# Kernel tuning notes

Measured on AMD Instinct MI355X. Metric: run time of the kernel, lower is better.

The kernel has to match this reference:

```python
import jax, jax.numpy as jnp
import numpy as np

B, LV, HW, LT, D, H = 4, 16, 196, 32, 768, 12
DH = D // H
SCALE = 1.0 / np.sqrt(DH).astype(np.float32)


def _lin(x, W, b):
    # torch nn.Linear convention: W is [out, in]
    return x @ W.T + b


def _split_heads(x):
    # (..., D) -> (..., H, DH)
    return x.reshape(*x.shape[:-1], H, DH)


def _attn_logits(feat_q, feat_k, mask_q, mask_k, Wq, bq, Wk, bk):
    # feat_q: (B, LV, Lq, D), feat_k: (B, LV, Lk, D)
    q = _split_heads(_lin(feat_q, Wq, bq))  # b v q h d
    k = _split_heads(_lin(feat_k, Wk, bk))  # b v k h d
    logits = jnp.einsum('bvqhd,bvkhd->bvhqk', q, k)
    m = (mask_q[:, :, None] & mask_k[:, None, :])[:, None, None]  # b 1 1 q k
    return jnp.where(m, logits, -10000.0)


def setup_inputs() -> dict:
    key = jax.random.key(0)
    ks = jax.random.split(key, 12)
    inp = {
        'vid_feat': jax.random.normal(ks[0], (B, LV, HW, D), jnp.float32),
        'txt_feat': jax.random.normal(ks[1], (B, LV, LT, D), jnp.float32),
        'vid_mask': jnp.ones((B, LV), dtype=bool),
        'txt_mask': jax.random.randint(ks[2], (B, LT), 0, 2) > 0,
    }
    for i, name in enumerate(['v2v', 't2v', 't2t', 'v2t']):
        inp[name + '_W'] = jax.random.normal(ks[3 + 2 * i], (3, D, D), jnp.float32) * 0.02
        inp[name + '_b'] = jnp.zeros((3, D), jnp.float32)
    return inp


def reference(vid_feat, txt_feat, vid_mask, txt_mask,
              v2v_W, v2v_b, t2v_W, t2v_b, t2t_W, t2t_b, v2t_W, v2t_b):
    mask_hw = jnp.ones((vid_feat.shape[0], HW), dtype=bool)

    # values: concat video-keys then text-keys along the key axis
    v_value = jnp.concatenate([_lin(vid_feat, v2v_W[2], v2v_b[2]),
                               _lin(txt_feat, t2v_W[2], t2v_b[2])], axis=2)
    v_value = _split_heads(v_value)  # b v (HW+LT) h d
    t_value = jnp.concatenate([_lin(vid_feat, v2t_W[2], v2t_b[2]),
                               _lin(txt_feat, t2t_W[2], t2t_b[2])], axis=2)
    t_value = _split_heads(t_value)

    # logits (source call order: get_attn_logits(feat_k, mask_k, feat_q, mask_q, ...))
    v2v = _attn_logits(vid_feat, vid_feat, mask_hw, mask_hw, v2v_W[0], v2v_b[0], v2v_W[1], v2v_b[1])
    t2v = _attn_logits(vid_feat, txt_feat, mask_hw, txt_mask, t2v_W[0], t2v_b[0], t2v_W[1], t2v_b[1])
    v2t = _attn_logits(txt_feat, vid_feat, txt_mask, mask_hw, v2t_W[0], v2t_b[0], v2t_W[1], v2t_b[1])
    t2t = _attn_logits(txt_feat, txt_feat, txt_mask, txt_mask, t2t_W[0], t2t_b[0], t2t_W[1], t2t_b[1])

    v_logits = jnp.concatenate([v2v, t2v], axis=-1)  # b v h HW (HW+LT)
    t_logits = jnp.concatenate([v2t, t2t], axis=-1)  # b v h LT (HW+LT)

    # NOTE: source scales probabilities AFTER softmax by 1/sqrt(d_head)
    vid_out = jnp.einsum('bvhqk,bvkhd->bvqhd', jax.nn.softmax(v_logits, axis=-1) * SCALE, v_value)
    vid_out = vid_out.reshape(*vid_out.shape[:3], D)
    txt_out = jnp.einsum('bvhqk,bvkhd->bvqhd', jax.nn.softmax(t_logits, axis=-1) * SCALE, t_value)
    txt_out = txt_out.reshape(*txt_out.shape[:3], D)
    return (vid_out, txt_out)
```

## Files before the change

kernel.cpp:

```cpp
#include <hip/hip_runtime.h>

#define NBV 64
#define HWN 196
#define LTN 32
#define DIM 768
#define NH 12
#define DHD 64
#define ATT_SCALE 0.125f

typedef __attribute__((ext_vector_type(8))) __bf16 bf16x8;
typedef __attribute__((ext_vector_type(4))) float f32x4;

static __device__ __forceinline__ unsigned short f2bf(float f) {
    union { float f; unsigned u; } v; v.f = f;
    unsigned r = v.u + 0x7FFFu + ((v.u >> 16) & 1u);
    return (unsigned short)(r >> 16);
}

#define MFMA16(a, b, c) __builtin_amdgcn_mfma_f32_16x16x32_bf16((a), (b), (c), 0, 0, 0)
#define GLOAD_LDS16(g, l)                                                      \
    __builtin_amdgcn_global_load_lds(                                          \
        (const __attribute__((address_space(1))) void*)(g),                    \
        (__attribute__((address_space(3))) void*)(l), 16, 0, 0)

struct CvtCfg {
    const float* src[14];
    unsigned short* dst[14];
    int n4[14];
};

__global__ __launch_bounds__(256) void cvt_bf16(CvtCfg cfg) {
    const int e = blockIdx.y;
    const float4* s = (const float4*)cfg.src[e];
    unsigned short* d = cfg.dst[e];
    const int n4 = cfg.n4[e];
    for (int i = blockIdx.x * 256 + threadIdx.x; i < n4; i += gridDim.x * 256) {
        float4 v = s[i];
        ushort4 o;
        o.x = f2bf(v.x); o.y = f2bf(v.y); o.z = f2bf(v.z); o.w = f2bf(v.w);
        *(ushort4*)(d + (long)i * 4) = o;
    }
}

struct BiasCfg { const float* b[6]; };

__global__ __launch_bounds__(512, 2) void gemm_proj(
    const unsigned short* __restrict__ A, const unsigned short* __restrict__ W,
    unsigned short* __restrict__ out, BiasCfg bias, int M)
{
    __shared__ __align__(16) unsigned short lds[65536];
    const int tid = threadIdx.x;
    const int lane = tid & 63, wid = tid >> 6;
    const int wm = wid >> 2, wn = wid & 3;
    const int fr = lane & 15, fg = lane >> 4;

    const int nwg = gridDim.x;
    const int orig = blockIdx.x;
    const int q = nwg >> 3, r = nwg & 7;
    const int xcd = orig & 7, lid = orig >> 3;
    const int wg = (xcd < r ? xcd * (q + 1) : r * (q + 1) + (xcd - r) * q) + lid;
    const int mt = wg / 18, nt = wg - mt * 18;
    const int m0 = mt * 256, n0 = nt * 256;

    const int srow = tid >> 2;
    const int sxor = ((tid & 3) ^ ((tid >> 3) & 3)) * 8;
    const unsigned short* aSrc = A + (long)(m0 + srow) * DIM + sxor;
    const unsigned short* bSrc = W + (long)(n0 + srow) * DIM + sxor;
    unsigned short* ldst = lds + tid * 8;

    const int rxor = (fg ^ ((fr >> 1) & 3)) * 8;
    const int aoff = (wm * 128 + fr) * 32 + rxor;
    const int boff = 8192 + (wn * 64 + fr) * 32 + rxor;

    f32x4 acc[8][4] = {};

#define STAGE(t, s) do {                                                       \
    const unsigned short* _a = aSrc + (t) * 32;                                \
    const unsigned short* _b = bSrc + (t) * 32;                                \
    unsigned short* _d = ldst + (s) * 16384;                                   \
    GLOAD_LDS16(_a, _d);                                                       \
    GLOAD_LDS16(_a + 98304, _d + 4096);                                        \
    GLOAD_LDS16(_b, _d + 8192);                                                \
    GLOAD_LDS16(_b + 98304, _d + 12288);                                       \
} while (0)

#define COMPUTE(s) do {                                                        \
    const unsigned short* _sa = lds + (s) * 16384 + aoff;                      \
    const unsigned short* _sb = lds + (s) * 16384 + boff;                      \
    bf16x8 af[8], bg[4];                                                       \
    _Pragma("unroll") for (int m = 0; m < 8; ++m)                              \
        af[m] = *(const bf16x8*)(_sa + m * 512);                               \
    _Pragma("unroll") for (int n = 0; n < 4; ++n)                              \
        bg[n] = *(const bf16x8*)(_sb + n * 512);                               \
    __builtin_amdgcn_s_setprio(1);                                             \
    _Pragma("unroll") for (int m = 0; m < 8; ++m)                              \
    _Pragma("unroll") for (int n = 0; n < 4; ++n)                              \
        acc[m][n] = MFMA16(af[m], bg[n], acc[m][n]);                           \
    __builtin_amdgcn_s_setprio(0);                                             \
} while (0)

    STAGE(0, 0); STAGE(1, 1); STAGE(2, 2);
#pragma unroll 1
    for (int t = 0; t < 21; ++t) {
        STAGE(t + 3, (t + 3) & 3);
        asm volatile("s_waitcnt vmcnt(12)" ::: "memory");
        __builtin_amdgcn_s_barrier();
        COMPUTE(t & 3);
        __builtin_amdgcn_s_barrier();
    }
    asm volatile("s_waitcnt vmcnt(8)" ::: "memory");
    __builtin_amdgcn_s_barrier();
    COMPUTE(1);
    asm volatile("s_waitcnt vmcnt(4)" ::: "memory");
    __builtin_amdgcn_s_barrier();
    COMPUTE(2);
    asm volatile("s_waitcnt vmcnt(0)" ::: "memory");
    __builtin_amdgcn_s_barrier();
    COMPUTE(3);

#undef STAGE
#undef COMPUTE

    const int w = nt / 3;
    const int nlb = (nt - w * 3) * 256;
    const float* bp = bias.b[w];
    unsigned short* op = out + (long)w * M * DIM;
#pragma unroll
    for (int n = 0; n < 4; ++n) {
        int gn = nlb + wn * 64 + n * 16 + fr;
        float bvl = bp[gn];
#pragma unroll
        for (int m = 0; m < 8; ++m) {
            int gmb = m0 + wm * 128 + m * 16 + fg * 4;
#pragma unroll
            for (int j = 0; j < 4; ++j)
                op[(long)(gmb + j) * DIM + gn] = f2bf(acc[m][n][j] + bvl);
        }
    }
}

__global__ __launch_bounds__(256) void transpose_v(
    const unsigned short* __restrict__ src, unsigned short* __restrict__ dst,
    int nrows, int colbase)
{
    __shared__ unsigned short t[32][33];
    const int bv = blockIdx.z, rt = blockIdx.x, dt = blockIdx.y;
    const int tx = threadIdx.x & 31, ty = threadIdx.x >> 5;
#pragma unroll
    for (int i = 0; i < 4; ++i) {
        int r = rt * 32 + ty + i * 8;
        t[ty + i * 8][tx] = (r < nrows)
            ? src[(long)(bv * nrows + r) * DIM + dt * 32 + tx] : (unsigned short)0;
    }
    __syncthreads();
#pragma unroll
    for (int i = 0; i < 4; ++i) {
        int d = dt * 32 + ty + i * 8;
        int rr = rt * 32 + tx;
        if (rr < nrows)
            dst[(long)(bv * DIM + d) * 256 + colbase + rr] = t[tx][ty + i * 8];
    }
}

__global__ __launch_bounds__(256, 2) void attn_kernel(
    const unsigned short* __restrict__ QA, const unsigned short* __restrict__ QB,
    const unsigned short* __restrict__ KV, const unsigned short* __restrict__ KT,
    const unsigned short* __restrict__ Vt, const int* __restrict__ tmask,
    float* __restrict__ outp, int nq, int qmask)
{
    __shared__ __align__(16) unsigned short P[4][16][256];
    const int tid = threadIdx.x, lane = tid & 63, wid = tid >> 6;
    const int bv = blockIdx.x, h = blockIdx.y;
    const int b = bv >> 4;
    const int q0 = blockIdx.z * 64 + wid * 16;
    const int fr = lane & 15, fg = lane >> 4;

    int qr = q0 + fr; if (qr > nq - 1) qr = nq - 1;
    const unsigned short* qa_p = QA + (long)(bv * nq + qr) * DIM + h * DHD;
    const unsigned short* qb_p = QB + (long)(bv * nq + qr) * DIM + h * DHD;
    bf16x8 qa[2], qb[2];
#pragma unroll
    for (int kh = 0; kh < 2; ++kh) {
        qa[kh] = *(const bf16x8*)(qa_p + kh * 32 + fg * 8);
        qb[kh] = *(const bf16x8*)(qb_p + kh * 32 + fg * 8);
    }

    f32x4 acc[15];
#pragma unroll
    for (int kb = 0; kb < 13; ++kb) {
        int kr = kb * 16 + fr; if (kr > HWN - 1) kr = HWN - 1;
        const unsigned short* kp = KV + (long)(bv * HWN + kr) * DIM + h * DHD;
        f32x4 c = {0.f, 0.f, 0.f, 0.f};
        c = MFMA16(qa[0], *(const bf16x8*)(kp + fg * 8), c);
        c = MFMA16(qa[1], *(const bf16x8*)(kp + 32 + fg * 8), c);
        acc[kb] = c;
    }
#pragma unroll
    for (int kb = 13; kb < 15; ++kb) {
        int kr = (kb - 13) * 16 + fr;
        const unsigned short* kp = KT + (long)(bv * LTN + kr) * DIM + h * DHD;
        f32x4 c = {0.f, 0.f, 0.f, 0.f};
        c = MFMA16(qb[0], *(const bf16x8*)(kp + fg * 8), c);
        c = MFMA16(qb[1], *(const bf16x8*)(kp + 32 + fg * 8), c);
        acc[kb] = c;
    }

    bool vq[4];
#pragma unroll
    for (int j = 0; j < 4; ++j) {
        int q = q0 + fg * 4 + j;
        if (qmask) { int qc = q < LTN ? q : LTN - 1; vq[j] = tmask[b * LTN + qc] != 0; }
        else vq[j] = true;
    }
#pragma unroll
    for (int kb = 0; kb < 15; ++kb) {
        int c = kb * 16 + fr;
        bool kreal = (c < HWN) || (c >= 208);
        bool kvalid = true;
        if (c >= 208) kvalid = tmask[b * LTN + (c - 208)] != 0;
#pragma unroll
        for (int j = 0; j < 4; ++j) {
            float l = acc[kb][j];
            if (!kreal) l = -3.0e38f;
            else if (!(kvalid && vq[j])) l = -10000.0f;
            acc[kb][j] = l;
        }
    }

    float mx[4], sm[4];
#pragma unroll
    for (int j = 0; j < 4; ++j) {
        float m = acc[0][j];
#pragma unroll
        for (int kb = 1; kb < 15; ++kb) m = fmaxf(m, acc[kb][j]);
        for (int s = 1; s < 16; s <<= 1) m = fmaxf(m, __shfl_xor(m, s, 64));
        mx[j] = m;
    }
#pragma unroll
    for (int j = 0; j < 4; ++j) {
        float s = 0.f;
#pragma unroll
        for (int kb = 0; kb < 15; ++kb) {
            float p = __expf(acc[kb][j] - mx[j]);
            acc[kb][j] = p;
            s += p;
        }
        for (int st = 1; st < 16; st <<= 1) s += __shfl_xor(s, st, 64);
        sm[j] = s;
    }

#pragma unroll
    for (int kb = 0; kb < 15; ++kb)
#pragma unroll
        for (int j = 0; j < 4; ++j)
            P[wid][fg * 4 + j][kb * 16 + fr] = f2bf(acc[kb][j]);
#pragma unroll
    for (int j = 0; j < 4; ++j)
        P[wid][fg * 4 + j][240 + fr] = 0;
    __syncthreads();

    f32x4 oacc[4] = {};
    const unsigned short* vt_base = Vt + (long)(bv * DIM + h * DHD) * 256;
#pragma unroll
    for (int ks = 0; ks < 8; ++ks) {
        bf16x8 a = *(const bf16x8*)&P[wid][fr][ks * 32 + fg * 8];
#pragma unroll
        for (int n = 0; n < 4; ++n) {
            const unsigned short* vp = vt_base + (long)(n * 16 + fr) * 256 + ks * 32 + fg * 8;
            oacc[n] = MFMA16(a, *(const bf16x8*)vp, oacc[n]);
        }
    }

#pragma unroll
    for (int n = 0; n < 4; ++n)
#pragma unroll
        for (int j = 0; j < 4; ++j) {
            int q = q0 + fg * 4 + j;
            if (q < nq)
                outp[(long)(bv * nq + q) * DIM + h * DHD + n * 16 + fr] =
                    oacc[n][j] * (ATT_SCALE / sm[j]);
        }
}

extern "C" void kernel_launch(void* const* d_in, const int* in_sizes, int n_in,
                              void* d_out, int out_size, void* d_ws, size_t ws_size,
                              hipStream_t stream)
{
    const float* vid_feat = (const float*)d_in[0];
    const float* txt_feat = (const float*)d_in[1];
    const int*   txt_mask = (const int*)d_in[3];
    const float* v2v_W = (const float*)d_in[4];
    const float* v2v_b = (const float*)d_in[5];
    const float* t2v_W = (const float*)d_in[6];
    const float* t2v_b = (const float*)d_in[7];
    const float* t2t_W = (const float*)d_in[8];
    const float* t2t_b = (const float*)d_in[9];
    const float* v2t_W = (const float*)d_in[10];
    const float* v2t_b = (const float*)d_in[11];

    char* ws = (char*)d_ws;
    unsigned short* vid_bf   = (unsigned short*)(ws);
    unsigned short* txt_bf   = (unsigned short*)(ws + 19267584L);
    unsigned short* Wv_bf    = (unsigned short*)(ws + 22413312L);
    unsigned short* Wt_bf    = (unsigned short*)(ws + 29491200L);
    unsigned short* proj_vid = (unsigned short*)(ws + 36569088L);
    unsigned short* proj_txt = (unsigned short*)(ws + 152174592L);
    unsigned short* Vt_v     = (unsigned short*)(ws + 171048960L);
    unsigned short* Vt_t     = (unsigned short*)(ws + 196214784L);

    const long WSL = 589824;
    CvtCfg cc;
    cc.src[0] = vid_feat; cc.dst[0] = vid_bf; cc.n4[0] = 9633792 / 4;
    cc.src[1] = txt_feat; cc.dst[1] = txt_bf; cc.n4[1] = 1572864 / 4;
    const float* wsrc_v[6] = { v2v_W, v2v_W + WSL, t2v_W, v2t_W + WSL,
                               v2v_W + 2 * WSL, v2t_W + 2 * WSL };
    const float* wsrc_t[6] = { t2v_W + WSL, t2v_W + 2 * WSL, v2t_W, t2t_W,
                               t2t_W + WSL, t2t_W + 2 * WSL };
    for (int i = 0; i < 6; ++i) {
        cc.src[2 + i] = wsrc_v[i]; cc.dst[2 + i] = Wv_bf + (long)i * WSL; cc.n4[2 + i] = WSL / 4;
        cc.src[8 + i] = wsrc_t[i]; cc.dst[8 + i] = Wt_bf + (long)i * WSL; cc.n4[8 + i] = WSL / 4;
    }
    cvt_bf16<<<dim3(2048, 14), 256, 0, stream>>>(cc);

    BiasCfg bvc, btc;
    const float* bsrc_v[6] = { v2v_b, v2v_b + 768, t2v_b, v2t_b + 768,
                               v2v_b + 1536, v2t_b + 1536 };
    const float* bsrc_t[6] = { t2v_b + 768, t2v_b + 1536, v2t_b, t2t_b,
                               t2t_b + 768, t2t_b + 1536 };
    for (int i = 0; i < 6; ++i) { bvc.b[i] = bsrc_v[i]; btc.b[i] = bsrc_t[i]; }

    gemm_proj<<<dim3(49 * 18), 512, 0, stream>>>(vid_bf, Wv_bf, proj_vid, bvc, 12544);
    gemm_proj<<<dim3(8 * 18), 512, 0, stream>>>(txt_bf, Wt_bf, proj_txt, btc, 2048);

    const long PV = 12544L * 768, PT = 2048L * 768;
    transpose_v<<<dim3(7, 24, 64), 256, 0, stream>>>(proj_vid + 4 * PV, Vt_v, 196, 0);
    transpose_v<<<dim3(1, 24, 64), 256, 0, stream>>>(proj_txt + 1 * PT, Vt_v, 32, 208);
    transpose_v<<<dim3(7, 24, 64), 256, 0, stream>>>(proj_vid + 5 * PV, Vt_t, 196, 0);
    transpose_v<<<dim3(1, 24, 64), 256, 0, stream>>>(proj_txt + 5 * PT, Vt_t, 32, 208);

    float* out_f = (float*)d_out;
    attn_kernel<<<dim3(64, 12, 4), 256, 0, stream>>>(
        proj_vid + 0 * PV, proj_vid + 2 * PV, proj_vid + 1 * PV, proj_txt + 0 * PT,
        Vt_v, txt_mask, out_f, 196, 0);
    attn_kernel<<<dim3(64, 12, 1), 256, 0, stream>>>(
        proj_txt + 2 * PT, proj_txt + 3 * PT, proj_vid + 3 * PV, proj_txt + 4 * PT,
        Vt_t, txt_mask, out_f + 9633792, 32, 1);
}
```

Measured before the change: 321.9 us.

## Merge GEMM, transpose and attention launches and restage GEMM epilogue via LDS

```diff
diff --git a/kernel.cpp b/kernel.cpp
--- a/kernel.cpp
+++ b/kernel.cpp
@@ -42,11 +42,15 @@
     }
 }
 
-struct BiasCfg { const float* b[6]; };
-
-__global__ __launch_bounds__(512, 2) void gemm_proj(
-    const unsigned short* __restrict__ A, const unsigned short* __restrict__ W,
-    unsigned short* __restrict__ out, BiasCfg bias, int M)
+struct GemmCfg {
+    const unsigned short* A[2];
+    const unsigned short* W[2];
+    unsigned short* out[2];
+    const float* bias[2][6];
+    int M[2];
+};
+
+__global__ __launch_bounds__(512, 2) void gemm_proj(GemmCfg cfg, int nb0)
 {
     __shared__ __align__(16) unsigned short lds[65536];
     const int tid = threadIdx.x;
@@ -59,8 +63,14 @@
     const int q = nwg >> 3, r = nwg & 7;
     const int xcd = orig & 7, lid = orig >> 3;
     const int wg = (xcd < r ? xcd * (q + 1) : r * (q + 1) + (xcd - r) * q) + lid;
-    const int mt = wg / 18, nt = wg - mt * 18;
+
+    const int set = wg >= nb0;
+    const int local = wg - (set ? nb0 : 0);
+    const int mt = local / 18, nt = local - mt * 18;
     const int m0 = mt * 256, n0 = nt * 256;
+    const int M = cfg.M[set];
+    const unsigned short* __restrict__ A = cfg.A[set];
+    const unsigned short* __restrict__ W = cfg.W[set];
 
     const int srow = tid >> 2;
     const int sxor = ((tid & 3) ^ ((tid >> 3) & 3)) * 8;
@@ -88,25 +98,31 @@
     const unsigned short* _sa = lds + (s) * 16384 + aoff;                      \
     const unsigned short* _sb = lds + (s) * 16384 + boff;                      \
     bf16x8 af[8], bg[4];                                                       \
-    _Pragma("unroll") for (int m = 0; m < 8; ++m)                              \
+    _Pragma("unroll") for (int m = 0; m < 4; ++m)                              \
         af[m] = *(const bf16x8*)(_sa + m * 512);                               \
     _Pragma("unroll") for (int n = 0; n < 4; ++n)                              \
         bg[n] = *(const bf16x8*)(_sb + n * 512);                               \
+    _Pragma("unroll") for (int m = 4; m < 8; ++m)                              \
+        af[m] = *(const bf16x8*)(_sa + m * 512);                               \
     __builtin_amdgcn_s_setprio(1);                                             \
-    _Pragma("unroll") for (int m = 0; m < 8; ++m)                              \
+    _Pragma("unroll") for (int m = 0; m < 4; ++m)                              \
     _Pragma("unroll") for (int n = 0; n < 4; ++n)                              \
-        acc[m][n] = MFMA16(af[m], bg[n], acc[m][n]);                           \
+        acc[m][n] = MFMA16(bg[n], af[m], acc[m][n]);                           \
+    __builtin_amdgcn_s_setprio(0);                                             \
+    __builtin_amdgcn_s_setprio(1);                                             \
+    _Pragma("unroll") for (int m = 4; m < 8; ++m)                              \
+    _Pragma("unroll") for (int n = 0; n < 4; ++n)                              \
+        acc[m][n] = MFMA16(bg[n], af[m], acc[m][n]);                           \
     __builtin_amdgcn_s_setprio(0);                                             \
 } while (0)
 
     STAGE(0, 0); STAGE(1, 1); STAGE(2, 2);
 #pragma unroll 1
     for (int t = 0; t < 21; ++t) {
+        asm volatile("s_waitcnt vmcnt(8)" ::: "memory");
+        __builtin_amdgcn_s_barrier();
         STAGE(t + 3, (t + 3) & 3);
-        asm volatile("s_waitcnt vmcnt(12)" ::: "memory");
-        __builtin_amdgcn_s_barrier();
         COMPUTE(t & 3);
-        __builtin_amdgcn_s_barrier();
     }
     asm volatile("s_waitcnt vmcnt(8)" ::: "memory");
     __builtin_amdgcn_s_barrier();
@@ -123,28 +139,58 @@
 
     const int w = nt / 3;
     const int nlb = (nt - w * 3) * 256;
-    const float* bp = bias.b[w];
-    unsigned short* op = out + (long)w * M * DIM;
-#pragma unroll
-    for (int n = 0; n < 4; ++n) {
-        int gn = nlb + wn * 64 + n * 16 + fr;
-        float bvl = bp[gn];
-#pragma unroll
-        for (int m = 0; m < 8; ++m) {
-            int gmb = m0 + wm * 128 + m * 16 + fg * 4;
-#pragma unroll
-            for (int j = 0; j < 4; ++j)
-                op[(long)(gmb + j) * DIM + gn] = f2bf(acc[m][n][j] + bvl);
-        }
-    }
-}
-
-__global__ __launch_bounds__(256) void transpose_v(
-    const unsigned short* __restrict__ src, unsigned short* __restrict__ dst,
-    int nrows, int colbase)
+    const float* bp = cfg.bias[set][w];
+    unsigned short* op = cfg.out[set] + (long)w * M * DIM;
+    const int colL = wn * 64;
+    __builtin_amdgcn_s_barrier();
+#pragma unroll
+    for (int p = 0; p < 2; ++p) {
+        if (wm == p) {
+#pragma unroll
+            for (int n = 0; n < 4; ++n) {
+                float4 b4 = *(const float4*)(bp + nlb + colL + n * 16 + fg * 4);
+#pragma unroll
+                for (int m = 0; m < 8; ++m) {
+                    ushort4 u;
+                    u.x = f2bf(acc[m][n][0] + b4.x);
+                    u.y = f2bf(acc[m][n][1] + b4.y);
+                    u.z = f2bf(acc[m][n][2] + b4.z);
+                    u.w = f2bf(acc[m][n][3] + b4.w);
+                    *(ushort4*)&lds[(m * 16 + fr) * 264 + colL + n * 16 + fg * 4] = u;
+                }
+            }
+        }
+        __builtin_amdgcn_s_barrier();
+#pragma unroll
+        for (int i = 0; i < 8; ++i) {
+            int chunk = tid + i * 512;
+            int rr = chunk >> 5, cb = chunk & 31;
+            bf16x8 v = *(const bf16x8*)&lds[rr * 264 + cb * 8];
+            *(bf16x8*)(op + (long)(m0 + p * 128 + rr) * DIM + nlb + cb * 8) = v;
+        }
+        if (p == 0) __builtin_amdgcn_s_barrier();
+    }
+}
+
+struct TransCfg {
+    const unsigned short* src[4];
+    unsigned short* dst[4];
+};
+
+__global__ __launch_bounds__(256) void transpose_v(TransCfg cfg)
 {
     __shared__ unsigned short t[32][33];
-    const int bv = blockIdx.z, rt = blockIdx.x, dt = blockIdx.y;
+    const int x = blockIdx.x;
+    const int which = x >> 3;
+    const int xi = x & 7;
+    const int istxt = (xi == 7);
+    const unsigned short* src = cfg.src[which * 2 + istxt];
+    unsigned short* dst = cfg.dst[which];
+    const int nrows = istxt ? LTN : HWN;
+    const int colbase = istxt ? 208 : 0;
+    const int rt = istxt ? 0 : xi;
+
+    const int bv = blockIdx.z, dt = blockIdx.y;
     const int tx = threadIdx.x & 31, ty = threadIdx.x >> 5;
 #pragma unroll
     for (int i = 0; i < 4; ++i) {
@@ -162,17 +208,32 @@
     }
 }
 
-__global__ __launch_bounds__(256, 2) void attn_kernel(
-    const unsigned short* __restrict__ QA, const unsigned short* __restrict__ QB,
-    const unsigned short* __restrict__ KV, const unsigned short* __restrict__ KT,
-    const unsigned short* __restrict__ Vt, const int* __restrict__ tmask,
-    float* __restrict__ outp, int nq, int qmask)
+struct AttnCfg {
+    const unsigned short* QA[2];
+    const unsigned short* QB[2];
+    const unsigned short* KV[2];
+    const unsigned short* KT[2];
+    const unsigned short* Vt[2];
+    float* outp[2];
+};
+
+__global__ __launch_bounds__(256, 2) void attn_kernel(AttnCfg cfg,
+                                                      const int* __restrict__ tmask)
 {
     __shared__ __align__(16) unsigned short P[4][16][256];
     const int tid = threadIdx.x, lane = tid & 63, wid = tid >> 6;
     const int bv = blockIdx.x, h = blockIdx.y;
     const int b = bv >> 4;
-    const int q0 = blockIdx.z * 64 + wid * 16;
+    const int sel = (blockIdx.z == 4);
+    const int nq = sel ? LTN : HWN;
+    const int qmask = sel;
+    const unsigned short* QA = cfg.QA[sel];
+    const unsigned short* QB = cfg.QB[sel];
+    const unsigned short* KV = cfg.KV[sel];
+    const unsigned short* KT = cfg.KT[sel];
+    const unsigned short* Vt = cfg.Vt[sel];
+    float* outp = cfg.outp[sel];
+    const int q0 = (sel ? 0 : blockIdx.z * 64) + wid * 16;
     const int fr = lane & 15, fg = lane >> 4;
 
     int qr = q0 + fr; if (qr > nq - 1) qr = nq - 1;
@@ -208,8 +269,8 @@
     bool vq[4];
 #pragma unroll
     for (int j = 0; j < 4; ++j) {
-        int q = q0 + fg * 4 + j;
-        if (qmask) { int qc = q < LTN ? q : LTN - 1; vq[j] = tmask[b * LTN + qc] != 0; }
+        int qq = q0 + fg * 4 + j;
+        if (qmask) { int qc = qq < LTN ? qq : LTN - 1; vq[j] = tmask[b * LTN + qc] != 0; }
         else vq[j] = true;
     }
 #pragma unroll
@@ -275,9 +336,9 @@
     for (int n = 0; n < 4; ++n)
 #pragma unroll
         for (int j = 0; j < 4; ++j) {
-            int q = q0 + fg * 4 + j;
-            if (q < nq)
-                outp[(long)(bv * nq + q) * DIM + h * DHD + n * 16 + fr] =
+            int qq = q0 + fg * 4 + j;
+            if (qq < nq)
+                outp[(long)(bv * nq + qq) * DIM + h * DHD + n * 16 + fr] =
                     oacc[n][j] * (ATT_SCALE / sm[j]);
         }
 }
@@ -322,27 +383,29 @@
     }
     cvt_bf16<<<dim3(2048, 14), 256, 0, stream>>>(cc);
 
-    BiasCfg bvc, btc;
+    GemmCfg gc;
+    gc.A[0] = vid_bf;  gc.W[0] = Wv_bf;  gc.out[0] = proj_vid;  gc.M[0] = 12544;
+    gc.A[1] = txt_bf;  gc.W[1] = Wt_bf;  gc.out[1] = proj_txt;  gc.M[1] = 2048;
     const float* bsrc_v[6] = { v2v_b, v2v_b + 768, t2v_b, v2t_b + 768,
                                v2v_b + 1536, v2t_b + 1536 };
     const float* bsrc_t[6] = { t2v_b + 768, t2v_b + 1536, v2t_b, t2t_b,
                                t2t_b + 768, t2t_b + 1536 };
-    for (int i = 0; i < 6; ++i) { bvc.b[i] = bsrc_v[i]; btc.b[i] = bsrc_t[i]; }
-
-    gemm_proj<<<dim3(49 * 18), 512, 0, stream>>>(vid_bf, Wv_bf, proj_vid, bvc, 12544);
-    gemm_proj<<<dim3(8 * 18), 512, 0, stream>>>(txt_bf, Wt_bf, proj_txt, btc, 2048);
+    for (int i = 0; i < 6; ++i) { gc.bias[0][i] = bsrc_v[i]; gc.bias[1][i] = bsrc_t[i]; }
+    gemm_proj<<<dim3(49 * 18 + 8 * 18), 512, 0, stream>>>(gc, 49 * 18);
 
     const long PV = 12544L * 768, PT = 2048L * 768;
-    transpose_v<<<dim3(7, 24, 64), 256, 0, stream>>>(proj_vid + 4 * PV, Vt_v, 196, 0);
-    transpose_v<<<dim3(1, 24, 64), 256, 0, stream>>>(proj_txt + 1 * PT, Vt_v, 32, 208);
-    transpose_v<<<dim3(7, 24, 64), 256, 0, stream>>>(proj_vid + 5 * PV, Vt_t, 196, 0);
-    transpose_v<<<dim3(1, 24, 64), 256, 0, stream>>>(proj_txt + 5 * PT, Vt_t, 32, 208);
+    TransCfg tc;
+    tc.src[0] = proj_vid + 4 * PV;  tc.src[1] = proj_txt + 1 * PT;  tc.dst[0] = Vt_v;
+    tc.src[2] = proj_vid + 5 * PV;  tc.src[3] = proj_txt + 5 * PT;  tc.dst[1] = Vt_t;
+    transpose_v<<<dim3(16, 24, 64), 256, 0, stream>>>(tc);
 
     float* out_f = (float*)d_out;
-    attn_kernel<<<dim3(64, 12, 4), 256, 0, stream>>>(
-        proj_vid + 0 * PV, proj_vid + 2 * PV, proj_vid + 1 * PV, proj_txt + 0 * PT,
-        Vt_v, txt_mask, out_f, 196, 0);
-    attn_kernel<<<dim3(64, 12, 1), 256, 0, stream>>>(
-        proj_txt + 2 * PT, proj_txt + 3 * PT, proj_vid + 3 * PV, proj_txt + 4 * PT,
-        Vt_t, txt_mask, out_f + 9633792, 32, 1);
-}
+    AttnCfg ac;
+    ac.QA[0] = proj_vid + 0 * PV;  ac.QB[0] = proj_vid + 2 * PV;
+    ac.KV[0] = proj_vid + 1 * PV;  ac.KT[0] = proj_txt + 0 * PT;
+    ac.Vt[0] = Vt_v;               ac.outp[0] = out_f;
+    ac.QA[1] = proj_txt + 2 * PT;  ac.QB[1] = proj_txt + 3 * PT;
+    ac.KV[1] = proj_vid + 3 * PV;  ac.KT[1] = proj_txt + 4 * PT;
+    ac.Vt[1] = Vt_t;               ac.outp[1] = out_f + 9633792;
+    attn_kernel<<<dim3(64, 12, 5), 256, 0, stream>>>(ac, txt_mask);
+}
```

Measured after the change: 302.3 us. -6.1%, faster.
